# Performance work log

Hardware: AMD Instinct MI355X
Metric: run time of the kernel (lower is better)

## Reference

```python
import jax, jax.numpy as jnp
import numpy as np

N = 2048      # quadrature nodes
C = 32        # lift_dim
DEPTH = 3
IN_FEATS = 2  # f_x feat (1) + grid coord (1)


def setup_inputs() -> dict:
    key = jax.random.key(0)
    ks = jax.random.split(key, 16)
    s = 0.1
    f_x = jax.random.normal(ks[0], (N, 1), dtype=jnp.float32)
    x_grid = jnp.sort(jax.random.uniform(ks[1], (N, 1), dtype=jnp.float32), axis=0)
    q_weights = jax.random.uniform(ks[2], (N, 1), dtype=jnp.float32) / N  # positive quadrature weights
    lift_W = jax.random.normal(ks[3], (C, IN_FEATS)) * (1.0 / np.sqrt(IN_FEATS))
    lift_b = jax.random.normal(ks[4], (C,)) * s
    pw_W = jax.random.normal(ks[5], (DEPTH, C, C)) * (1.0 / np.sqrt(C))   # Conv1d(k=1) weights
    pw_b = jax.random.normal(ks[6], (DEPTH, C)) * s
    ker_log_ell = jax.random.normal(ks[7], (DEPTH, C)) * 0.1 - 1.0        # per-channel RBF lengthscale (log)
    ker_log_sigma = jax.random.normal(ks[8], (DEPTH, C)) * 0.1            # per-channel RBF amplitude (log)
    proj1_W = jax.random.normal(ks[9], (C, C)) * (1.0 / np.sqrt(C))
    proj1_b = jax.random.normal(ks[10], (C,)) * s
    proj2_W = jax.random.normal(ks[11], (C, C)) * (1.0 / np.sqrt(C))
    proj2_b = jax.random.normal(ks[12], (C,)) * s
    proj3_W = jax.random.normal(ks[13], (1, C)) * (1.0 / np.sqrt(C))
    proj3_b = jax.random.normal(ks[14], (1,)) * s
    return {"f_x": f_x, "x_grid": x_grid, "q_weights": q_weights,
            "lift_W": lift_W, "lift_b": lift_b, "pw_W": pw_W, "pw_b": pw_b,
            "ker_log_ell": ker_log_ell, "ker_log_sigma": ker_log_sigma,
            "proj1_W": proj1_W, "proj1_b": proj1_b, "proj2_W": proj2_W,
            "proj2_b": proj2_b, "proj3_W": proj3_W, "proj3_b": proj3_b}


def reference(f_x, x_grid, q_weights, lift_W, lift_b, pw_W, pw_b,
              ker_log_ell, ker_log_sigma, proj1_W, proj1_b,
              proj2_W, proj2_b, proj3_W, proj3_b):
    act = jax.nn.gelu
    # lift: concat(f, grid) -> [N, C]
    fq = act(jnp.concatenate([f_x, x_grid], axis=-1) @ lift_W.T + lift_b)
    x = x_grid[:, 0]                       # [N]
    w = q_weights[:, 0]                    # [N]
    d2 = (x[:, None] - x[None, :]) ** 2    # [N, N] pairwise squared distances
    depth = pw_W.shape[0]
    for i in range(depth):
        # pointwise 1x1 conv skip: [N, C]
        skip = fq @ pw_W[i].T + pw_b[i]
        # per-channel learned RBF kernel over all NxN node pairs: [C, N, N]
        ell2 = jnp.exp(2.0 * ker_log_ell[i])     # [C]
        sig2 = jnp.exp(2.0 * ker_log_sigma[i])   # [C]
        K = sig2[:, None, None] * jnp.exp(-d2[None, :, :] / (2.0 * ell2[:, None, None]))
        # quadrature-weighted integral transform: out[n,c] = sum_q K[c,n,q] * w[q] * f[q,c]
        integ = jnp.einsum('cnq,qc->nc', K, fq * w[:, None])
        fq = skip + integ
        if i < depth - 1:
            fq = act(fq)
    fq = act(fq @ proj1_W.T + proj1_b)
    fq = act(fq @ proj2_W.T + proj2_b)
    fq = fq @ proj3_W.T + proj3_b          # [N, 1]
    return fq.squeeze()
```

## Files before the change

### kernel.cpp

```cpp
#include <hip/hip_runtime.h>

#define NPTS 2048
#define CH 32
#define KT 32
#define NBLK 32
#define NTHR 512
#define RPB 64
#define LOG2E 1.4426950408889634f
#define MAGIC(l) (0x6B1D9C00 + (l))
#define WSOFF (16u << 20)

#if defined(__has_builtin)
#if __has_builtin(__builtin_amdgcn_exp2f)
#define EXP2F(x) __builtin_amdgcn_exp2f(x)
#endif
#endif
#ifndef EXP2F
#define EXP2F(x) exp2f(x)
#endif

struct Params {
    const float *f_x, *x_grid, *qw, *lift_W, *lift_b, *pw_W, *pw_b, *kle, *kls;
    const float *p1W, *p1b, *p2W, *p2b, *p3W, *p3b;
    int* ctrl;
    float* P;
    float* out;
};

__device__ __forceinline__ float gelu_tanh(float x) {
    float x3 = x * x * x;
    float u = 0.7978845608028654f * (x + 0.044715f * x3);
    return 0.5f * x * (1.0f + tanhf(u));
}

__global__ __launch_bounds__(NTHR, 1) void k_fused(Params p) {
    __shared__ float sWt[3][CH][CH];
    __shared__ float sW1t[CH][CH], sW2t[CH][CH];
    __shared__ float sb1[CH], sb2[CH], sW3v[CH], sbias[3][CH];
    __shared__ float xrow[RPB], wrow[RPB], lx[RPB];
    __shared__ float lgk[KT];
    __shared__ float fqb[2][RPB][CH];
    __shared__ float sS[RPB][CH];
    __shared__ float sM[KT][CH];

    const int tid = threadIdx.x;
    const int b = blockIdx.x;
    const int c = tid & 31;
    const int r0 = tid >> 5;
    const int n0 = b * RPB;

    for (int i = tid; i < 3 * CH * CH; i += NTHR) {
        const int l = i >> 10, cc = (i >> 5) & 31, k = i & 31;
        sWt[l][k][cc] = p.pw_W[i];
    }
    for (int i = tid; i < CH * CH; i += NTHR) {
        const int cc = i >> 5, k = i & 31;
        sW1t[k][cc] = p.p1W[i];
        sW2t[k][cc] = p.p2W[i];
    }
    if (tid < CH) { sb1[tid] = p.p1b[tid]; sb2[tid] = p.p2b[tid]; sW3v[tid] = p.p3W[tid]; }
    if (tid >= 64 && tid < 64 + 3 * CH) sbias[(tid - 64) >> 5][(tid - 64) & 31] = p.pw_b[tid - 64];
    if (tid < KT) lgk[tid] = lgammaf((float)tid + 1.0f) * LOG2E;
    if (tid < RPB) {
        const float xq = p.x_grid[n0 + tid];
        xrow[tid] = xq;
        wrow[tid] = p.qw[n0 + tid];
        lx[tid] = log2f(fmaxf(xq, 1e-30f));
    }
    __syncthreads();

    float nb2a[3], sig2a[3], lia[3];
#pragma unroll
    for (int l = 0; l < 3; l++) {
        const float invl2 = expf(-2.0f * p.kle[l * CH + c]);
        nb2a[l] = -0.5f * invl2 * LOG2E;
        sig2a[l] = expf(2.0f * p.kls[l * CH + c]);
        lia[l] = log2f(invl2);
    }

#pragma unroll
    for (int j = 0; j < 4; j++) {
        const int rr = r0 + 16 * j;
        float v = p.f_x[n0 + rr] * p.lift_W[c * 2] + xrow[rr] * p.lift_W[c * 2 + 1] + p.lift_b[c];
        fqb[0][rr][c] = gelu_tanh(v);
    }

    int cur = 0;
    for (int l = 0; l < 3; l++) {
#pragma unroll
        for (int j = 0; j < 4; j++) {
            const int rr = r0 + 16 * j;
            const float xq = xrow[rr];
            sS[rr][c] = EXP2F(xq * xq * nb2a[l]) * fqb[cur][rr][c] * wrow[rr];
        }
        __syncthreads();

        float* Pb = p.P + l * (NBLK * KT * CH) + b * (KT * CH);
        {
            const int k0 = tid >> 5, k1 = k0 + 16;
            const float kf0 = (float)k0, kf1 = (float)k1;
            const float nl0 = fmaf(kf0, lia[l], -lgk[k0]);
            const float nl1 = fmaf(kf1, lia[l], -lgk[k1]);
            float a0 = 0.0f, a1 = 0.0f;
#pragma unroll 16
            for (int rr = 0; rr < RPB; rr++) {
                const float s = sS[rr][c], lxr = lx[rr];
                a0 += EXP2F(fmaf(kf0, lxr, nl0)) * s;
                a1 += EXP2F(fmaf(kf1, lxr, nl1)) * s;
            }
            __hip_atomic_store(&Pb[k0 * CH + c], a0, __ATOMIC_RELAXED, __HIP_MEMORY_SCOPE_AGENT);
            __hip_atomic_store(&Pb[k1 * CH + c], a1, __ATOMIC_RELAXED, __HIP_MEMORY_SCOPE_AGENT);
        }

        float skip[4];
#pragma unroll
        for (int j = 0; j < 4; j++) skip[j] = sbias[l][c];
#pragma unroll
        for (int k = 0; k < CH; k++) {
            const float wv = sWt[l][k][c];
#pragma unroll
            for (int j = 0; j < 4; j++)
                skip[j] = fmaf(fqb[cur][r0 + 16 * j][k], wv, skip[j]);
        }

        int* flags = p.ctrl + l * 32;
        __syncthreads();
        if (tid == 0)
            __hip_atomic_store(flags + b, MAGIC(l), __ATOMIC_RELAXED, __HIP_MEMORY_SCOPE_AGENT);
        if (tid < 64) {
            for (;;) {
                const int v = __hip_atomic_load(flags + (tid & 31),
                                                __ATOMIC_RELAXED, __HIP_MEMORY_SCOPE_AGENT);
                if (__all(v == MAGIC(l))) break;
                __builtin_amdgcn_s_sleep(1);
            }
        }
        __syncthreads();

        {
            const unsigned long long* P0 =
                (const unsigned long long*)(p.P + l * (NBLK * KT * CH));
            float ax = 0.0f, ay = 0.0f;
#pragma unroll
            for (int h = 0; h < 2; h++) {
                unsigned long long v[16];
#pragma unroll
                for (int u = 0; u < 16; u++)
                    v[u] = __hip_atomic_load(P0 + (h * 16 + u) * (KT * CH / 2) + tid,
                                             __ATOMIC_RELAXED, __HIP_MEMORY_SCOPE_AGENT);
#pragma unroll
                for (int u = 0; u < 16; u++) {
                    union { unsigned long long q; float f[2]; } cv; cv.q = v[u];
                    ax += cv.f[0]; ay += cv.f[1];
                }
            }
            sM[tid >> 4][(2 * tid) & 31] = ax;
            sM[tid >> 4][(2 * tid + 1) & 31] = ay;
        }
        __syncthreads();

        {
            float Ph[4];
#pragma unroll
            for (int j = 0; j < 4; j++) Ph[j] = sM[KT - 1][c];
#pragma unroll
            for (int k = KT - 2; k >= 0; k--) {
                const float mk = sM[k][c];
#pragma unroll
                for (int j = 0; j < 4; j++) Ph[j] = fmaf(Ph[j], xrow[r0 + 16 * j], mk);
            }
#pragma unroll
            for (int j = 0; j < 4; j++) {
                const int rr = r0 + 16 * j;
                const float xn = xrow[rr];
                float v = skip[j] + sig2a[l] * EXP2F(xn * xn * nb2a[l]) * Ph[j];
                if (l < 2) v = gelu_tanh(v);
                fqb[cur ^ 1][rr][c] = v;
            }
        }
        cur ^= 1;
    }
    __syncthreads();

#pragma unroll
    for (int j = 0; j < 4; j++) {
        const int rr = r0 + 16 * j;
        float s = sb1[c];
#pragma unroll
        for (int k = 0; k < CH; k++) s = fmaf(fqb[cur][rr][k], sW1t[k][c], s);
        sS[rr][c] = gelu_tanh(s);
    }
    __syncthreads();
#pragma unroll
    for (int j = 0; j < 4; j++) {
        const int rr = r0 + 16 * j;
        float s = sb2[c];
#pragma unroll
        for (int k = 0; k < CH; k++) s = fmaf(sS[rr][k], sW2t[k][c], s);
        fqb[0][rr][c] = gelu_tanh(s);
    }
    __syncthreads();
    if (tid < RPB) {
        float s = p.p3b[0];
#pragma unroll
        for (int k = 0; k < CH; k++) s = fmaf(fqb[0][tid][k], sW3v[k], s);
        p.out[n0 + tid] = s;
    }
}

extern "C" void kernel_launch(void* const* d_in, const int* in_sizes, int n_in,
                              void* d_out, int out_size, void* d_ws, size_t ws_size,
                              hipStream_t stream) {
    Params p;
    p.f_x    = (const float*)d_in[0];
    p.x_grid = (const float*)d_in[1];
    p.qw     = (const float*)d_in[2];
    p.lift_W = (const float*)d_in[3];
    p.lift_b = (const float*)d_in[4];
    p.pw_W   = (const float*)d_in[5];
    p.pw_b   = (const float*)d_in[6];
    p.kle    = (const float*)d_in[7];
    p.kls    = (const float*)d_in[8];
    p.p1W    = (const float*)d_in[9];
    p.p1b    = (const float*)d_in[10];
    p.p2W    = (const float*)d_in[11];
    p.p2b    = (const float*)d_in[12];
    p.p3W    = (const float*)d_in[13];
    p.p3b    = (const float*)d_in[14];

    p.ctrl   = (int*)((char*)d_ws + WSOFF);
    p.P      = (float*)((char*)d_ws + WSOFF + 4096);
    p.out    = (float*)d_out;

    k_fused<<<dim3(NBLK), dim3(NTHR), 0, stream>>>(p);
}
```

Baseline: 33.63 us.

## Replace block-level grid barrier with per-wave flags and fuse layer prologue

Each wave now signals its own flag as soon as its partial moments are written, and every wave polls all per-wave flags itself. This removes the two __syncthreads that surrounded the single-thread flag handshake, so waves no longer wait for the whole block before entering the cross-block wait. The weighted input for the next layer is now computed in the previous layer's epilogue, which drops one barrier per layer. The cost is more polling traffic, since every wave of every block spins on 256 flags, and the ordering between the data stores and the flag store now relies on an explicit vmcnt wait rather than a block barrier.

```diff
diff --git a/kernel.cpp b/kernel.cpp
--- a/kernel.cpp
+++ b/kernel.cpp
@@ -7,7 +7,7 @@
 #define NTHR 512
 #define RPB 64
 #define LOG2E 1.4426950408889634f
-#define MAGIC(l) (0x6B1D9C00 + (l))
+#define MAGICV(l) (0x6B1D9C00 + (l))
 #define WSOFF (16u << 20)
 
 #if defined(__has_builtin)
@@ -48,6 +48,8 @@
     const int c = tid & 31;
     const int r0 = tid >> 5;
     const int n0 = b * RPB;
+    const int wv = tid >> 6;
+    const int lane = tid & 63;
 
     for (int i = tid; i < 3 * CH * CH; i += NTHR) {
         const int l = i >> 10, cc = (i >> 5) & 31, k = i & 31;
@@ -82,18 +84,16 @@
     for (int j = 0; j < 4; j++) {
         const int rr = r0 + 16 * j;
         float v = p.f_x[n0 + rr] * p.lift_W[c * 2] + xrow[rr] * p.lift_W[c * 2 + 1] + p.lift_b[c];
-        fqb[0][rr][c] = gelu_tanh(v);
-    }
-
-    int cur = 0;
+        v = gelu_tanh(v);
+        fqb[0][rr][c] = v;
+        const float xq = xrow[rr];
+        sS[rr][c] = EXP2F(xq * xq * nb2a[0]) * v * wrow[rr];
+    }
+    __syncthreads();
+
+#pragma unroll
     for (int l = 0; l < 3; l++) {
-#pragma unroll
-        for (int j = 0; j < 4; j++) {
-            const int rr = r0 + 16 * j;
-            const float xq = xrow[rr];
-            sS[rr][c] = EXP2F(xq * xq * nb2a[l]) * fqb[cur][rr][c] * wrow[rr];
-        }
-        __syncthreads();
+        const int cur = l & 1, nxt = cur ^ 1;
 
         float* Pb = p.P + l * (NBLK * KT * CH) + b * (KT * CH);
         {
@@ -112,30 +112,36 @@
             __hip_atomic_store(&Pb[k1 * CH + c], a1, __ATOMIC_RELAXED, __HIP_MEMORY_SCOPE_AGENT);
         }
 
+        int* flags = p.ctrl + l * 256;
+        asm volatile("s_waitcnt vmcnt(0)" ::: "memory");
+        if (lane == 0)
+            __hip_atomic_store(flags + b * 8 + wv, MAGICV(l),
+                               __ATOMIC_RELAXED, __HIP_MEMORY_SCOPE_AGENT);
+
         float skip[4];
 #pragma unroll
         for (int j = 0; j < 4; j++) skip[j] = sbias[l][c];
 #pragma unroll
         for (int k = 0; k < CH; k++) {
-            const float wv = sWt[l][k][c];
+            const float wvv = sWt[l][k][c];
 #pragma unroll
             for (int j = 0; j < 4; j++)
-                skip[j] = fmaf(fqb[cur][r0 + 16 * j][k], wv, skip[j]);
-        }
-
-        int* flags = p.ctrl + l * 32;
-        __syncthreads();
-        if (tid == 0)
-            __hip_atomic_store(flags + b, MAGIC(l), __ATOMIC_RELAXED, __HIP_MEMORY_SCOPE_AGENT);
-        if (tid < 64) {
+                skip[j] = fmaf(fqb[cur][r0 + 16 * j][k], wvv, skip[j]);
+        }
+
+        {
+            const unsigned long long mm =
+                ((unsigned long long)(unsigned)MAGICV(l) << 32) | (unsigned)MAGICV(l);
+            const unsigned long long* F = (const unsigned long long*)flags;
             for (;;) {
-                const int v = __hip_atomic_load(flags + (tid & 31),
+                const unsigned long long f0 = __hip_atomic_load(F + lane * 2,
                                                 __ATOMIC_RELAXED, __HIP_MEMORY_SCOPE_AGENT);
-                if (__all(v == MAGIC(l))) break;
+                const unsigned long long f1 = __hip_atomic_load(F + lane * 2 + 1,
+                                                __ATOMIC_RELAXED, __HIP_MEMORY_SCOPE_AGENT);
+                if (__all(f0 == mm && f1 == mm)) break;
                 __builtin_amdgcn_s_sleep(1);
             }
         }
-        __syncthreads();
 
         {
             const unsigned long long* P0 =
@@ -174,20 +180,22 @@
                 const int rr = r0 + 16 * j;
                 const float xn = xrow[rr];
                 float v = skip[j] + sig2a[l] * EXP2F(xn * xn * nb2a[l]) * Ph[j];
-                if (l < 2) v = gelu_tanh(v);
-                fqb[cur ^ 1][rr][c] = v;
-            }
-        }
-        cur ^= 1;
-    }
-    __syncthreads();
+                if (l < 2) {
+                    v = gelu_tanh(v);
+                    sS[rr][c] = EXP2F(xn * xn * nb2a[l + 1]) * v * wrow[rr];
+                }
+                fqb[nxt][rr][c] = v;
+            }
+        }
+        __syncthreads();
+    }
 
 #pragma unroll
     for (int j = 0; j < 4; j++) {
         const int rr = r0 + 16 * j;
         float s = sb1[c];
 #pragma unroll
-        for (int k = 0; k < CH; k++) s = fmaf(fqb[cur][rr][k], sW1t[k][c], s);
+        for (int k = 0; k < CH; k++) s = fmaf(fqb[1][rr][k], sW1t[k][c], s);
         sS[rr][c] = gelu_tanh(s);
     }
     __syncthreads();
@@ -229,7 +237,7 @@
     p.p3b    = (const float*)d_in[14];
 
     p.ctrl   = (int*)((char*)d_ws + WSOFF);
-    p.P      = (float*)((char*)d_ws + WSOFF + 4096);
+    p.P      = (float*)((char*)d_ws + WSOFF + 8192);
     p.out    = (float*)d_out;
 
     k_fused<<<dim3(NBLK), dim3(NTHR), 0, stream>>>(p);
```

Result: no change. 33.72 us (+0.3%).
